# Optimization experiments

Hardware: AMD Instinct MI355X
Metric: run time of the kernel (lower is better)

The kernel has to match this reference:

```python
import jax, jax.numpy as jnp
import numpy as np

B, IN_DIM, HID, S = 131072, 8, 32, 16
ERR_THR = 0.01          # QuantumErrorCorrection.error_threshold
ENT_STRENGTH = 0.4      # config.quantum_entanglement_strength
EULER_DT = 0.1


def setup_inputs() -> dict:
    key = jax.random.key(0)
    ks = jax.random.split(key, 7)
    x = jax.random.normal(ks[0], (B, IN_DIM), dtype=jnp.float32)
    h_quantum = jax.random.normal(ks[1], (B, HID, S), dtype=jnp.float32)
    quantum_weights = jax.random.normal(ks[2], (IN_DIM, HID, S), dtype=jnp.float32) * 0.1
    recurrent_weights = jax.random.normal(ks[3], (HID, HID, S), dtype=jnp.float32) * 0.1
    base_tau = jax.random.uniform(ks[4], (HID,), dtype=jnp.float32, minval=1.0, maxval=50.0)
    syndrome_matrix = jax.random.normal(ks[5], (4, S), dtype=jnp.float32)
    correction_weights = jax.random.normal(ks[6], (4, S), dtype=jnp.float32) * 0.1
    return {"x": x, "h_quantum": h_quantum, "quantum_weights": quantum_weights,
            "recurrent_weights": recurrent_weights, "base_tau": base_tau,
            "syndrome_matrix": syndrome_matrix, "correction_weights": correction_weights}


def reference(x, h_quantum, quantum_weights, recurrent_weights, base_tau,
              syndrome_matrix, correction_weights):
    # --- quantum error correction (thresholded syndrome correction) ---
    # syndrome: [B, H, C]
    syndrome = jnp.einsum('bhs,cs->bhc', h_quantum, syndrome_matrix)
    masked_syndrome = jnp.where(jnp.abs(syndrome) > ERR_THR, syndrome, 0.0)
    h_q = h_quantum - jnp.einsum('bhc,cs->bhs', masked_syndrome, correction_weights)

    # --- liquid ODE update, fused over all superposition states ---
    # adaptation_factor = 1.0 (OPTIMAL health, no performance stats)
    tau = base_tau[None, :, None]                              # [1, H, 1]
    inp = jnp.einsum('bi,ihs->bhs', x, quantum_weights)        # [B, H, S]
    rec = jnp.einsum('bhs,hks->bks', h_q, recurrent_weights)   # [B, H, S]
    activation = jnp.tanh(inp + rec)                           # no fault detected -> tanh path
    new_q = h_q + EULER_DT * (-h_q / tau + activation)

    # --- nearest-neighbor entanglement between adjacent states ---
    coupling = ENT_STRENGTH * new_q[:, :, :-1] * new_q[:, :, 1:]       # [B, H, S-1]
    ent = (jnp.pad(coupling, ((0, 0), (0, 0), (0, 1)))
           + jnp.pad(coupling, ((0, 0), (0, 0), (1, 0))))
    stable = new_q + 0.1 * ent
    norms = jnp.linalg.norm(stable, axis=1, keepdims=True)             # [B, 1, S]
    q_norm = stable / (norms + 1e-8)

    # --- adaptive measurement (QUANTUM_OPTIMIZED -> balanced branch) ---
    energy = jnp.sum(q_norm ** 2, axis=1, keepdims=True)               # [B, 1, S]
    magnitude = jnp.sum(jnp.abs(q_norm), axis=1, keepdims=True)        # [B, 1, S]
    probs = magnitude / (energy + 1e-6)
    probs = probs / jnp.sum(probs, axis=-1, keepdims=True)
    output = jnp.sum(q_norm * probs, axis=-1)                          # [B, H]
    return (output, q_norm)
```

## Files before the change

### kernel.cpp

```cpp
#include <hip/hip_runtime.h>

typedef __attribute__((ext_vector_type(8))) __bf16 bf16x8;
typedef __attribute__((ext_vector_type(8))) unsigned short us8;
typedef __attribute__((ext_vector_type(4))) float f32x4;

#define NB 16
#define B_TOTAL 131072
#define SST 36
#define BST 580

__device__ __forceinline__ unsigned short f2bf(float f) {
  union { float f; unsigned int u; } c; c.f = f;
  unsigned int u = c.u;
  u += 0x7fffu + ((u >> 16) & 1u);
  return (unsigned short)(u >> 16);
}
__device__ __forceinline__ bf16x8 as_bf(us8 v) {
  union { us8 u; bf16x8 b; } c; c.u = v; return c.b;
}
__device__ __forceinline__ float fast_tanh(float x) {
  float t = __expf(2.0f * x);
  return 1.0f - 2.0f / (t + 1.0f);
}

__global__ void shq_prep(const float* __restrict__ qw, const float* __restrict__ rw,
                         const float* __restrict__ tau,
                         unsigned short* __restrict__ rwfrag,
                         unsigned short* __restrict__ qwfrag,
                         unsigned short* __restrict__ dgfrag) {
  int g = blockIdx.x * 256 + threadIdx.x;
  if (g < 2048) {
    int s = g >> 7, kh = (g >> 6) & 1, ln = g & 63;
    int k = kh * 16 + (ln & 15), h0 = (ln >> 4) * 8;
    us8 v;
#pragma unroll
    for (int e = 0; e < 8; ++e) v[e] = f2bf(rw[((h0 + e) * 32 + k) * 16 + s]);
    *(us8*)(rwfrag + g * 8) = v;
  } else if (g < 2560) {
    int j = g - 2048;
    int s = j >> 5, kh = (j >> 4) & 1, ln = j & 15;
    int hc = kh * 16 + ln;
    us8 v;
#pragma unroll
    for (int e = 0; e < 8; ++e) v[e] = f2bf(qw[(e * 32 + hc) * 16 + s]);
    *(us8*)(qwfrag + j * 8) = v;
  } else if (g < 2688) {
    int j = g - 2560;
    int kh = (j >> 6) & 1, ln = j & 63;
    int k = kh * 16 + (ln & 15), h0 = (ln >> 4) * 8;
    unsigned short ab = f2bf(1.0f - 0.1f / tau[k]);
    us8 v;
#pragma unroll
    for (int e = 0; e < 8; ++e) v[e] = (h0 + e == k) ? ab : (unsigned short)0;
    *(us8*)(dgfrag + j * 8) = v;
  }
}

__global__ __launch_bounds__(512, 4) void shq_main(
    const float* __restrict__ x, const float* __restrict__ hq_g,
    const float* __restrict__ syn, const float* __restrict__ corr,
    const unsigned short* __restrict__ rwfrag,
    const unsigned short* __restrict__ qwfrag,
    const unsigned short* __restrict__ dgfrag,
    float* __restrict__ out) {
  __shared__ float smem[16 * BST];
  __shared__ float2 lds_pi[NB * 16];
  unsigned short* hqT = (unsigned short*)smem;

  const int tid = threadIdx.x;
  const int b0 = blockIdx.x * NB;
  const int lane = tid & 63;
  const int w = tid >> 6;

  us8 z8 = {0, 0, 0, 0, 0, 0, 0, 0};

  us8 xu = z8;
  if (lane < 16) {
    const float* xb = x + (size_t)(b0 + lane) * 8;
    f32x4 a = *(const f32x4*)xb, b = *(const f32x4*)(xb + 4);
    xu[0] = f2bf(a[0]); xu[1] = f2bf(a[1]); xu[2] = f2bf(a[2]); xu[3] = f2bf(a[3]);
    xu[4] = f2bf(b[0]); xu[5] = f2bf(b[1]); xu[6] = f2bf(b[2]); xu[7] = f2bf(b[3]);
  }

  {
    const int bl = tid >> 5, hh = tid & 31;
    const float* hb = hq_g + (((size_t)(b0 + bl) * 32) + hh) * 16;
    f32x4 h0 = *(const f32x4*)(hb), h1 = *(const f32x4*)(hb + 4);
    f32x4 h2 = *(const f32x4*)(hb + 8), h3 = *(const f32x4*)(hb + 12);
    float hrow[16];
#pragma unroll
    for (int q = 0; q < 4; ++q) {
      hrow[0 + q] = h0[q]; hrow[4 + q] = h1[q]; hrow[8 + q] = h2[q]; hrow[12 + q] = h3[q];
    }
    float sd[4];
#pragma unroll
    for (int c = 0; c < 4; ++c) {
      float a = 0.f;
#pragma unroll
      for (int s = 0; s < 16; ++s) a = fmaf(hrow[s], syn[c * 16 + s], a);
      sd[c] = (fabsf(a) > 0.01f) ? a : 0.f;
    }
#pragma unroll
    for (int s = 0; s < 16; ++s) {
      float cs = sd[0] * corr[s] + sd[1] * corr[16 + s] + sd[2] * corr[32 + s] + sd[3] * corr[48 + s];
      hqT[s * 640 + bl * 40 + hh] = f2bf(hrow[s] - cs);
    }
  }
  __syncthreads();

  us8 hq_u[2];
#pragma unroll
  for (int sl = 0; sl < 2; ++sl)
    hq_u[sl] = *(const us8*)&hqT[(2 * w + sl) * 640 + (lane & 15) * 40 + (lane >> 4) * 8];
  us8 dg0 = *(const us8*)(dgfrag + lane * 8);
  us8 dg1 = *(const us8*)(dgfrag + (64 + lane) * 8);
  __syncthreads();

  {
    f32x4 zro = {0.f, 0.f, 0.f, 0.f};
#pragma unroll
    for (int sl = 0; sl < 2; ++sl) {
      int s = 2 * w + sl;
      bf16x8 hqf = as_bf(hq_u[sl]);
#pragma unroll
      for (int kh = 0; kh < 2; ++kh) {
        us8 rwv = *(const us8*)(rwfrag + ((s * 2 + kh) * 64 + lane) * 8);
        us8 qwv = (lane < 16) ? *(const us8*)(qwfrag + ((s * 2 + kh) * 16 + lane) * 8) : z8;
        f32x4 acc = __builtin_amdgcn_mfma_f32_16x16x32_bf16(as_bf(xu), as_bf(qwv), zro, 0, 0, 0);
        acc = __builtin_amdgcn_mfma_f32_16x16x32_bf16(hqf, as_bf(rwv), acc, 0, 0, 0);
        f32x4 na;
#pragma unroll
        for (int r = 0; r < 4; ++r) na[r] = 0.1f * fast_tanh(acc[r]);
        na = __builtin_amdgcn_mfma_f32_16x16x32_bf16(hqf, as_bf(kh ? dg1 : dg0), na, 0, 0, 0);
        int k = kh * 16 + (lane & 15);
#pragma unroll
        for (int r = 0; r < 4; ++r) {
          int br = (lane >> 4) * 4 + r;
          smem[br * BST + s * SST + k] = na[r];
        }
      }
    }
  }
  __syncthreads();

  {
    int b3 = tid >> 5, idx = tid & 31;
    int s3 = idx >> 1, half = idx & 1;
    int base = b3 * BST + s3 * SST + half * 16;
    float ssq = 0.f, sab = 0.f;
    f32x4 zv = {0.f, 0.f, 0.f, 0.f};
#pragma unroll
    for (int q = 0; q < 4; ++q) {
      f32x4 c0 = *(const f32x4*)&smem[base + 4 * q];
      f32x4 cm = (s3 > 0)  ? *(const f32x4*)&smem[base - SST + 4 * q] : zv;
      f32x4 cp = (s3 < 15) ? *(const f32x4*)&smem[base + SST + 4 * q] : zv;
#pragma unroll
      for (int e = 0; e < 4; ++e) {
        float st = fmaf(0.04f * c0[e], cm[e] + cp[e], c0[e]);
        ssq = fmaf(st, st, ssq);
        sab += fabsf(st);
      }
    }
    ssq += __shfl_xor(ssq, 1);
    sab += __shfl_xor(sab, 1);
    float inv = __fdividef(1.0f, sqrtf(ssq) + 1e-8f);
    float energy = ssq * inv * inv;
    float mag = sab * inv;
    float pu = __fdividef(mag, energy + 1e-6f);
    float psum = pu;
#pragma unroll
    for (int m = 2; m < 32; m <<= 1) psum += __shfl_xor(psum, m);
    if (half == 0) {
      float2 pv = {__fdividef(pu, psum), inv};
      lds_pi[b3 * 16 + s3] = pv;
    }
  }
  __syncthreads();

  {
    const int b3 = tid >> 5, h3 = tid & 31;
    const float* colp = smem + b3 * BST + h3;
    float* qp = out + 4194304 + (((size_t)(b0 + b3) * 32) + h3) * 16;
    float prev = 0.f;
    float cur = colp[0];
    float oacc = 0.f;
    f32x4 qbuf;
#pragma unroll
    for (int s = 0; s < 16; ++s) {
      float nxt = (s < 15) ? colp[(s + 1) * SST] : 0.f;
      float st = fmaf(0.04f * cur, prev + nxt, cur);
      float2 pv = lds_pi[b3 * 16 + s];
      float q = st * pv.y;
      qbuf[s & 3] = q;
      oacc = fmaf(q, pv.x, oacc);
      if ((s & 3) == 3) *(f32x4*)(qp + (s - 3)) = qbuf;
      prev = cur; cur = nxt;
    }
    out[(size_t)(b0 + b3) * 32 + h3] = oacc;
  }
}

extern "C" void kernel_launch(void* const* d_in, const int* in_sizes, int n_in,
                              void* d_out, int out_size, void* d_ws, size_t ws_size,
                              hipStream_t stream) {
  const float* x    = (const float*)d_in[0];
  const float* hq   = (const float*)d_in[1];
  const float* qw   = (const float*)d_in[2];
  const float* rw   = (const float*)d_in[3];
  const float* tau  = (const float*)d_in[4];
  const float* syn  = (const float*)d_in[5];
  const float* corr = (const float*)d_in[6];
  unsigned short* ws = (unsigned short*)d_ws;
  unsigned short* rwfrag = ws;
  unsigned short* qwfrag = ws + 16384;
  unsigned short* dgfrag = ws + 20480;
  shq_prep<<<11, 256, 0, stream>>>(qw, rw, tau, rwfrag, qwfrag, dgfrag);
  shq_main<<<B_TOTAL / NB, 512, 0, stream>>>(x, hq, syn, corr, rwfrag, qwfrag, dgfrag, (float*)d_out);
}
```

Before: 153.8 us.

## Move whole per-batch pipeline into one wave's registers, dropping LDS and barriers

Each wavefront now owns 16 batch rows end to end. It loads h_quantum straight into registers in MFMA fragment layout, keeps all 16 state slices of the ODE result in registers, and does the norm and probability reductions with lane shuffles instead of LDS staging and block barriers. Blocks shrink to 256 threads covering 64 batches, with launch bounds of 2 blocks per CU. The aim is to remove LDS round trips and __syncthreads. The cost is very high register pressure (hq[8][4], nq[2][16], frag[16]), which risks spills and low occupancy, plus many shuffles. Global access patterns for the hq loads and q_norm stores also change.

```diff
diff --git a/kernel.cpp b/kernel.cpp
--- a/kernel.cpp
+++ b/kernel.cpp
@@ -4,10 +4,7 @@
 typedef __attribute__((ext_vector_type(8))) unsigned short us8;
 typedef __attribute__((ext_vector_type(4))) float f32x4;
 
-#define NB 16
 #define B_TOTAL 131072
-#define SST 36
-#define BST 580
 
 __device__ __forceinline__ unsigned short f2bf(float f) {
   union { float f; unsigned int u; } c; c.f = f;
@@ -56,147 +53,152 @@
   }
 }
 
-__global__ __launch_bounds__(512, 4) void shq_main(
+__global__ __launch_bounds__(256, 2) void shq_main(
     const float* __restrict__ x, const float* __restrict__ hq_g,
     const float* __restrict__ syn, const float* __restrict__ corr,
     const unsigned short* __restrict__ rwfrag,
     const unsigned short* __restrict__ qwfrag,
     const unsigned short* __restrict__ dgfrag,
     float* __restrict__ out) {
-  __shared__ float smem[16 * BST];
-  __shared__ float2 lds_pi[NB * 16];
-  unsigned short* hqT = (unsigned short*)smem;
-
   const int tid = threadIdx.x;
-  const int b0 = blockIdx.x * NB;
   const int lane = tid & 63;
-  const int w = tid >> 6;
+  const size_t b0 = ((size_t)blockIdx.x * 4 + (tid >> 6)) * 16;
+  const int g = lane >> 4;
+  const int bi = lane & 15;
 
   us8 z8 = {0, 0, 0, 0, 0, 0, 0, 0};
 
-  us8 xu = z8;
-  if (lane < 16) {
-    const float* xb = x + (size_t)(b0 + lane) * 8;
-    f32x4 a = *(const f32x4*)xb, b = *(const f32x4*)(xb + 4);
-    xu[0] = f2bf(a[0]); xu[1] = f2bf(a[1]); xu[2] = f2bf(a[2]); xu[3] = f2bf(a[3]);
-    xu[4] = f2bf(b[0]); xu[5] = f2bf(b[1]); xu[6] = f2bf(b[2]); xu[7] = f2bf(b[3]);
-  }
-
+  f32x4 hq[8][4];
   {
-    const int bl = tid >> 5, hh = tid & 31;
-    const float* hb = hq_g + (((size_t)(b0 + bl) * 32) + hh) * 16;
-    f32x4 h0 = *(const f32x4*)(hb), h1 = *(const f32x4*)(hb + 4);
-    f32x4 h2 = *(const f32x4*)(hb + 8), h3 = *(const f32x4*)(hb + 12);
-    float hrow[16];
-#pragma unroll
-    for (int q = 0; q < 4; ++q) {
-      hrow[0 + q] = h0[q]; hrow[4 + q] = h1[q]; hrow[8 + q] = h2[q]; hrow[12 + q] = h3[q];
-    }
-    float sd[4];
+    const float* hb = hq_g + ((b0 + bi) * 32 + (size_t)g * 8) * 16;
+#pragma unroll
+    for (int e = 0; e < 8; ++e)
+#pragma unroll
+      for (int c = 0; c < 4; ++c)
+        hq[e][c] = *(const f32x4*)(hb + e * 16 + c * 4);
+  }
+  float sd[8][4];
+#pragma unroll
+  for (int e = 0; e < 8; ++e)
 #pragma unroll
     for (int c = 0; c < 4; ++c) {
       float a = 0.f;
 #pragma unroll
-      for (int s = 0; s < 16; ++s) a = fmaf(hrow[s], syn[c * 16 + s], a);
-      sd[c] = (fabsf(a) > 0.01f) ? a : 0.f;
-    }
+      for (int s = 0; s < 16; ++s) a = fmaf(hq[e][s >> 2][s & 3], syn[c * 16 + s], a);
+      sd[e][c] = (fabsf(a) > 0.01f) ? a : 0.f;
+    }
+  bf16x8 frag[16];
+#pragma unroll
+  for (int s = 0; s < 16; ++s) {
+#pragma unroll
+    for (int e = 0; e < 8; ++e) {
+      float cs = fmaf(sd[e][0], corr[s],
+                 fmaf(sd[e][1], corr[16 + s],
+                 fmaf(sd[e][2], corr[32 + s], sd[e][3] * corr[48 + s])));
+      frag[s][e] = (__bf16)(hq[e][s >> 2][s & 3] - cs);
+    }
+  }
+
+  bf16x8 xf = as_bf(z8);
+  if (g == 0) {
+    const float* xb = x + (b0 + bi) * 8;
+    f32x4 a = *(const f32x4*)xb, bv = *(const f32x4*)(xb + 4);
+#pragma unroll
+    for (int e = 0; e < 4; ++e) { xf[e] = (__bf16)a[e]; xf[e + 4] = (__bf16)bv[e]; }
+  }
+  bf16x8 dgf0 = as_bf(*(const us8*)(dgfrag + lane * 8));
+  bf16x8 dgf1 = as_bf(*(const us8*)(dgfrag + (64 + lane) * 8));
+
+  f32x4 nq[2][16];
+  const f32x4 zro = {0.f, 0.f, 0.f, 0.f};
+#pragma unroll
+  for (int s = 0; s < 16; ++s) {
+#pragma unroll
+    for (int kh = 0; kh < 2; ++kh) {
+      bf16x8 rwv = as_bf(*(const us8*)(rwfrag + ((s * 2 + kh) * 64 + lane) * 8));
+      bf16x8 qwv = (g == 0) ? as_bf(*(const us8*)(qwfrag + ((s * 2 + kh) * 16 + bi) * 8))
+                            : as_bf(z8);
+      f32x4 acc = __builtin_amdgcn_mfma_f32_16x16x32_bf16(xf, qwv, zro, 0, 0, 0);
+      acc = __builtin_amdgcn_mfma_f32_16x16x32_bf16(frag[s], rwv, acc, 0, 0, 0);
+      f32x4 na;
+#pragma unroll
+      for (int r = 0; r < 4; ++r) na[r] = 0.1f * fast_tanh(acc[r]);
+      nq[kh][s] = __builtin_amdgcn_mfma_f32_16x16x32_bf16(frag[s], dgf0 , na, 0, 0, 0);
+      if (kh) nq[1][s] = __builtin_amdgcn_mfma_f32_16x16x32_bf16(frag[s], dgf1, na, 0, 0, 0);
+      else    nq[0][s] = __builtin_amdgcn_mfma_f32_16x16x32_bf16(frag[s], dgf0, na, 0, 0, 0);
+    }
+  }
+
+  float ssqk[4], sabk[4];
+#pragma unroll
+  for (int s = 0; s < 16; ++s) {
+    float ssq[4], sab[4];
+#pragma unroll
+    for (int r = 0; r < 4; ++r) {
+      float c0 = nq[0][s][r], c1 = nq[1][s][r];
+      float nb0 = ((s > 0) ? nq[0][s - 1][r] : 0.f) + ((s < 15) ? nq[0][s + 1][r] : 0.f);
+      float nb1 = ((s > 0) ? nq[1][s - 1][r] : 0.f) + ((s < 15) ? nq[1][s + 1][r] : 0.f);
+      float st0 = fmaf(0.04f * c0, nb0, c0);
+      float st1 = fmaf(0.04f * c1, nb1, c1);
+      ssq[r] = fmaf(st0, st0, st1 * st1);
+      sab[r] = fabsf(st0) + fabsf(st1);
+    }
+#pragma unroll
+    for (int m = 1; m < 16; m <<= 1)
+#pragma unroll
+      for (int r = 0; r < 4; ++r) {
+        ssq[r] += __shfl_xor(ssq[r], m);
+        sab[r] += __shfl_xor(sab[r], m);
+      }
+    if (bi == s) {
+#pragma unroll
+      for (int r = 0; r < 4; ++r) { ssqk[r] = ssq[r]; sabk[r] = sab[r]; }
+    }
+  }
+  float invk[4], puk[4], prk[4];
+#pragma unroll
+  for (int r = 0; r < 4; ++r) {
+    float inv = __fdividef(1.f, sqrtf(ssqk[r]) + 1e-8f);
+    invk[r] = inv;
+    puk[r] = __fdividef(sabk[r] * inv, fmaf(ssqk[r] * inv, inv, 1e-6f));
+  }
+  {
+    float ps[4] = {puk[0], puk[1], puk[2], puk[3]};
+#pragma unroll
+    for (int m = 1; m < 16; m <<= 1)
+#pragma unroll
+      for (int r = 0; r < 4; ++r) ps[r] += __shfl_xor(ps[r], m);
+#pragma unroll
+    for (int r = 0; r < 4; ++r) prk[r] = __fdividef(puk[r], ps[r]);
+  }
+
+  float* qbase = out + 4194304;
+#pragma unroll
+  for (int r = 0; r < 4; ++r) {
+    const size_t bb = b0 + g * 4 + r;
+    float* qp0 = qbase + (bb * 32 + bi) * 16;
+    float* qp1 = qbase + (bb * 32 + 16 + bi) * 16;
+    float oa0 = 0.f, oa1 = 0.f;
+    f32x4 q0v, q1v;
 #pragma unroll
     for (int s = 0; s < 16; ++s) {
-      float cs = sd[0] * corr[s] + sd[1] * corr[16 + s] + sd[2] * corr[32 + s] + sd[3] * corr[48 + s];
-      hqT[s * 640 + bl * 40 + hh] = f2bf(hrow[s] - cs);
-    }
-  }
-  __syncthreads();
-
-  us8 hq_u[2];
-#pragma unroll
-  for (int sl = 0; sl < 2; ++sl)
-    hq_u[sl] = *(const us8*)&hqT[(2 * w + sl) * 640 + (lane & 15) * 40 + (lane >> 4) * 8];
-  us8 dg0 = *(const us8*)(dgfrag + lane * 8);
-  us8 dg1 = *(const us8*)(dgfrag + (64 + lane) * 8);
-  __syncthreads();
-
-  {
-    f32x4 zro = {0.f, 0.f, 0.f, 0.f};
-#pragma unroll
-    for (int sl = 0; sl < 2; ++sl) {
-      int s = 2 * w + sl;
-      bf16x8 hqf = as_bf(hq_u[sl]);
-#pragma unroll
-      for (int kh = 0; kh < 2; ++kh) {
-        us8 rwv = *(const us8*)(rwfrag + ((s * 2 + kh) * 64 + lane) * 8);
-        us8 qwv = (lane < 16) ? *(const us8*)(qwfrag + ((s * 2 + kh) * 16 + lane) * 8) : z8;
-        f32x4 acc = __builtin_amdgcn_mfma_f32_16x16x32_bf16(as_bf(xu), as_bf(qwv), zro, 0, 0, 0);
-        acc = __builtin_amdgcn_mfma_f32_16x16x32_bf16(hqf, as_bf(rwv), acc, 0, 0, 0);
-        f32x4 na;
-#pragma unroll
-        for (int r = 0; r < 4; ++r) na[r] = 0.1f * fast_tanh(acc[r]);
-        na = __builtin_amdgcn_mfma_f32_16x16x32_bf16(hqf, as_bf(kh ? dg1 : dg0), na, 0, 0, 0);
-        int k = kh * 16 + (lane & 15);
-#pragma unroll
-        for (int r = 0; r < 4; ++r) {
-          int br = (lane >> 4) * 4 + r;
-          smem[br * BST + s * SST + k] = na[r];
-        }
+      float inv = __shfl(invk[r], s, 16);
+      float pr  = __shfl(prk[r], s, 16);
+      float c0 = nq[0][s][r], c1 = nq[1][s][r];
+      float nb0 = ((s > 0) ? nq[0][s - 1][r] : 0.f) + ((s < 15) ? nq[0][s + 1][r] : 0.f);
+      float nb1 = ((s > 0) ? nq[1][s - 1][r] : 0.f) + ((s < 15) ? nq[1][s + 1][r] : 0.f);
+      float q0 = fmaf(0.04f * c0, nb0, c0) * inv;
+      float q1 = fmaf(0.04f * c1, nb1, c1) * inv;
+      q0v[s & 3] = q0; q1v[s & 3] = q1;
+      oa0 = fmaf(q0, pr, oa0);
+      oa1 = fmaf(q1, pr, oa1);
+      if ((s & 3) == 3) {
+        *(f32x4*)(qp0 + (s - 3)) = q0v;
+        *(f32x4*)(qp1 + (s - 3)) = q1v;
       }
     }
-  }
-  __syncthreads();
-
-  {
-    int b3 = tid >> 5, idx = tid & 31;
-    int s3 = idx >> 1, half = idx & 1;
-    int base = b3 * BST + s3 * SST + half * 16;
-    float ssq = 0.f, sab = 0.f;
-    f32x4 zv = {0.f, 0.f, 0.f, 0.f};
-#pragma unroll
-    for (int q = 0; q < 4; ++q) {
-      f32x4 c0 = *(const f32x4*)&smem[base + 4 * q];
-      f32x4 cm = (s3 > 0)  ? *(const f32x4*)&smem[base - SST + 4 * q] : zv;
-      f32x4 cp = (s3 < 15) ? *(const f32x4*)&smem[base + SST + 4 * q] : zv;
-#pragma unroll
-      for (int e = 0; e < 4; ++e) {
-        float st = fmaf(0.04f * c0[e], cm[e] + cp[e], c0[e]);
-        ssq = fmaf(st, st, ssq);
-        sab += fabsf(st);
-      }
-    }
-    ssq += __shfl_xor(ssq, 1);
-    sab += __shfl_xor(sab, 1);
-    float inv = __fdividef(1.0f, sqrtf(ssq) + 1e-8f);
-    float energy = ssq * inv * inv;
-    float mag = sab * inv;
-    float pu = __fdividef(mag, energy + 1e-6f);
-    float psum = pu;
-#pragma unroll
-    for (int m = 2; m < 32; m <<= 1) psum += __shfl_xor(psum, m);
-    if (half == 0) {
-      float2 pv = {__fdividef(pu, psum), inv};
-      lds_pi[b3 * 16 + s3] = pv;
-    }
-  }
-  __syncthreads();
-
-  {
-    const int b3 = tid >> 5, h3 = tid & 31;
-    const float* colp = smem + b3 * BST + h3;
-    float* qp = out + 4194304 + (((size_t)(b0 + b3) * 32) + h3) * 16;
-    float prev = 0.f;
-    float cur = colp[0];
-    float oacc = 0.f;
-    f32x4 qbuf;
-#pragma unroll
-    for (int s = 0; s < 16; ++s) {
-      float nxt = (s < 15) ? colp[(s + 1) * SST] : 0.f;
-      float st = fmaf(0.04f * cur, prev + nxt, cur);
-      float2 pv = lds_pi[b3 * 16 + s];
-      float q = st * pv.y;
-      qbuf[s & 3] = q;
-      oacc = fmaf(q, pv.x, oacc);
-      if ((s & 3) == 3) *(f32x4*)(qp + (s - 3)) = qbuf;
-      prev = cur; cur = nxt;
-    }
-    out[(size_t)(b0 + b3) * 32 + h3] = oacc;
+    out[bb * 32 + bi] = oa0;
+    out[bb * 32 + 16 + bi] = oa1;
   }
 }
 
@@ -215,5 +217,5 @@
   unsigned short* qwfrag = ws + 16384;
   unsigned short* dgfrag = ws + 20480;
   shq_prep<<<11, 256, 0, stream>>>(qw, rw, tau, rwfrag, qwfrag, dgfrag);
-  shq_main<<<B_TOTAL / NB, 512, 0, stream>>>(x, hq, syn, corr, rwfrag, qwfrag, dgfrag, (float*)d_out);
-}
+  shq_main<<<B_TOTAL / 64, 256, 0, stream>>>(x, hq, syn, corr, rwfrag, qwfrag, dgfrag, (float*)d_out);
+}
```

Result: slower. 250.4 us (+62.8%).
